# Performance work log

Measured on AMD Instinct MI355X. Metric: run time of the kernel, lower is better.

## Reference

```python
import jax, jax.numpy as jnp
import numpy as np
from functools import partial

VOCAB, D, H, L, T_MAX = 32000, 1024, 16, 8, 1024
HD = D // H
HIDDEN = int(D * 2.67)  # 2734, matches int(n_embd*hidden_mult)


def setup_inputs() -> dict:
    key = jax.random.key(0)
    ks = jax.random.split(key, 9)
    s = 0.02
    return {
        "idx": jax.random.randint(ks[0], (2, 1024), 0, VOCAB),
        "W_emb": jax.random.normal(ks[1], (VOCAB, D), jnp.float32) * s,  # tied with lm_head
        "norm1_w": jnp.ones((L, D), jnp.float32),
        "Wqkv": jax.random.normal(ks[2], (L, D, 3 * D), jnp.float32) * s,
        "Wout": jax.random.normal(ks[3], (L, D, D), jnp.float32) * s,
        "norm2_w": jnp.ones((L, D), jnp.float32),
        "Wg": jax.random.normal(ks[4], (L, D, HIDDEN), jnp.float32) * s,
        "Wu": jax.random.normal(ks[5], (L, D, HIDDEN), jnp.float32) * s,
        "Wd": jax.random.normal(ks[6], (L, HIDDEN, D), jnp.float32) * s,
        "final_norm_w": jnp.ones((D,), jnp.float32),
    }


def _rmsnorm(x, w, eps=1e-6):
    rms = jnp.sqrt(jnp.mean(x * x, axis=-1, keepdims=True) + eps)
    return x / rms * w


def _rope(x, cos_f, sin_f):
    # x: [B,H,T,hd]; cos_f/sin_f: [T, hd//2]
    x1, x2 = x[..., : HD // 2], x[..., HD // 2 :]
    c = cos_f[None, None]
    s = sin_f[None, None]
    return jnp.concatenate([x1 * c - x2 * s, x1 * s + x2 * c], axis=-1)


def _forward(idx, W_emb, norm1_w, Wqkv, Wout, norm2_w, Wg, Wu, Wd, final_norm_w):
    B, T = idx.shape
    # RoPE tables (buffers in the torch module)
    inv_freq = 1.0 / (10000.0 ** (jnp.arange(0, HD, 2, dtype=jnp.float32) / HD))
    ang = jnp.arange(T, dtype=jnp.float32)[:, None] * inv_freq[None, :]  # [T, hd//2]
    cos_f, sin_f = jnp.cos(ang), jnp.sin(ang)
    causal = jnp.tril(jnp.ones((T, T), dtype=bool))  # [T,T]
    scale = 1.0 / jnp.sqrt(jnp.float32(HD))

    def block(x, params):
        n1, wqkv, wout, n2, wg, wu, wd = params
        h = _rmsnorm(x, n1)
        qkv = (h @ wqkv).reshape(B, T, 3, H, HD).transpose(2, 0, 3, 1, 4)  # [3,B,H,T,hd]
        q, k, v = qkv[0], qkv[1], qkv[2]
        q = _rope(q, cos_f, sin_f)
        k = _rope(k, cos_f, sin_f)
        attn = jnp.einsum("bhqd,bhkd->bhqk", q, k) * scale
        attn = jnp.where(causal[None, None], attn, -jnp.inf)
        attn = jax.nn.softmax(attn, axis=-1)
        o = jnp.einsum("bhqk,bhkd->bhqd", attn, v)
        o = o.transpose(0, 2, 1, 3).reshape(B, T, D) @ wout
        x = x + o
        h2 = _rmsnorm(x, n2)
        x = x + (jax.nn.silu(h2 @ wg) * (h2 @ wu)) @ wd
        return x, None

    x = W_emb[idx]  # [B,T,D]
    x, _ = jax.lax.scan(block, x, (norm1_w, Wqkv, Wout, norm2_w, Wg, Wu, Wd))
    x = _rmsnorm(x, final_norm_w)
    return x @ W_emb.T  # tied lm_head -> [B,T,VOCAB]


def reference(idx, W_emb, norm1_w, Wqkv, Wout, norm2_w, Wg, Wu, Wd, final_norm_w):
    return _forward(idx, W_emb, norm1_w, Wqkv, Wout, norm2_w, Wg, Wu, Wd, final_norm_w)
```

## Files before the change

kernel.cpp:

```cpp
#include <hip/hip_runtime.h>
#include <cstdint>
#include <cmath>

#define D_MODEL 1024
#define T_SEQ   1024
#define NHEAD   16
#define NLAYER  8
#define HID     2734
#define HID_PAD 2816
#define NTOK    2048
#define VOCAB   32000

typedef __bf16 bf16x8 __attribute__((ext_vector_type(8)));
typedef __bf16 bf16x4 __attribute__((ext_vector_type(4)));
typedef float  f32x4  __attribute__((ext_vector_type(4)));

__device__ inline bf16x4 to_bf4(float a, float b, float c, float d) {
  bf16x4 t; t[0] = (__bf16)a; t[1] = (__bf16)b; t[2] = (__bf16)c; t[3] = (__bf16)d; return t;
}

__device__ inline void gload16(const __bf16* g, __bf16* l) {
  __builtin_amdgcn_global_load_lds(
      (const __attribute__((address_space(1))) void*)g,
      (__attribute__((address_space(3))) void*)l, 16, 0, 0);
}

__global__ __launch_bounds__(256) void embed_kernel(const int* __restrict__ idx,
                                                    const float* __restrict__ W,
                                                    float* __restrict__ x) {
  int t = blockIdx.x;
  int v = idx[t];
  float4 val = *(const float4*)&W[(size_t)v * D_MODEL + threadIdx.x * 4];
  *(float4*)&x[(size_t)t * D_MODEL + threadIdx.x * 4] = val;
}

__global__ __launch_bounds__(256) void rmsnorm_kernel(const float* __restrict__ x,
                                                      const float* __restrict__ w,
                                                      __bf16* __restrict__ out) {
  int row = blockIdx.x;
  int tid = threadIdx.x;
  float4 v = *(const float4*)&x[(size_t)row * D_MODEL + tid * 4];
  float s = v.x * v.x + v.y * v.y + v.z * v.z + v.w * v.w;
#pragma unroll
  for (int m = 32; m >= 1; m >>= 1) s += __shfl_xor(s, m, 64);
  __shared__ float red[4];
  if ((tid & 63) == 0) red[tid >> 6] = s;
  __syncthreads();
  float tot = red[0] + red[1] + red[2] + red[3];
  float inv = rsqrtf(tot * (1.0f / (float)D_MODEL) + 1e-6f);
  float4 wv = *(const float4*)&w[tid * 4];
  bf16x4 o4 = to_bf4(v.x * inv * wv.x, v.y * inv * wv.y, v.z * inv * wv.z, v.w * inv * wv.w);
  *(bf16x4*)&out[(size_t)row * D_MODEL + tid * 4] = o4;
}

__global__ __launch_bounds__(256) void rope_table_kernel(float* __restrict__ tab) {
  int p = blockIdx.x * 256 + threadIdx.x;
  int t = p >> 5, i = p & 31;
  float freq = exp2f(-(float)i * (13.287712379549449f / 32.0f));
  float sn, cs;
  sincosf((float)t * freq, &sn, &cs);
  tab[p] = cs;
  tab[32768 + p] = sn;
}

__global__ __launch_bounds__(256) void tp5_kernel(
    const float* __restrict__ Wqkv, const float* __restrict__ Wout,
    const float* __restrict__ Wg, const float* __restrict__ Wu,
    const float* __restrict__ Wd,
    __bf16* __restrict__ wqkvT, __bf16* __restrict__ woutT,
    __bf16* __restrict__ wguT, __bf16* __restrict__ wdT) {
  __shared__ __bf16 tile[64][65];
  int t = blockIdx.x;
  const float* in;
  __bf16* out;
  int R, C, Ro, rmul, roff, tr;
  if (t < 768)        { in = Wqkv; out = wqkvT; R = 1024; C = 3072; Ro = 1024; rmul = 1; roff = 0; tr = 16; }
  else if (t < 1024)  { t -= 768;  in = Wout; out = woutT; R = 1024; C = 1024; Ro = 1024; rmul = 1; roff = 0; tr = 16; }
  else if (t < 1728)  { t -= 1024; in = Wg; out = wguT; R = 1024; C = HID; Ro = 1024; rmul = 2; roff = 0; tr = 16; }
  else if (t < 2432)  { t -= 1728; in = Wu; out = wguT; R = 1024; C = HID; Ro = 1024; rmul = 2; roff = 1; tr = 16; }
  else                { t -= 2432; in = Wd; out = wdT; R = HID; C = 1024; Ro = HID_PAD; rmul = 1; roff = 0; tr = 44; }
  int r0 = (t % tr) * 64, c0 = (t / tr) * 64;
  int tid = threadIdx.x;
  bool fullc = (c0 + 64 <= C);
#pragma unroll
  for (int i = 0; i < 4; ++i) {
    int ri = i * 16 + (tid >> 4);
    int ci = (tid & 15) * 4;
    int r = r0 + ri;
    float4 v = {0.f, 0.f, 0.f, 0.f};
    if (r < R) {
      const float* p = in + (size_t)r * C + c0 + ci;
      if (fullc) {
        v = *(const float4*)p;
      } else {
        int c = c0 + ci;
        if (c + 0 < C) v.x = p[0];
        if (c + 1 < C) v.y = p[1];
        if (c + 2 < C) v.z = p[2];
        if (c + 3 < C) v.w = p[3];
      }
    }
    tile[ri][ci + 0] = (__bf16)v.x;
    tile[ri][ci + 1] = (__bf16)v.y;
    tile[ri][ci + 2] = (__bf16)v.z;
    tile[ri][ci + 3] = (__bf16)v.w;
  }
  __syncthreads();
#pragma unroll
  for (int i = 0; i < 4; ++i) {
    int oc = i * 16 + (tid >> 4);
    int orr = (tid & 15) * 4;
    bf16x4 tv;
    tv[0] = tile[orr + 0][oc];
    tv[1] = tile[orr + 1][oc];
    tv[2] = tile[orr + 2][oc];
    tv[3] = tile[orr + 3][oc];
    *(bf16x4*)&out[((size_t)(c0 + oc) * rmul + roff) * Ro + r0 + orr] = tv;
  }
}

__global__ __launch_bounds__(256) void convert_bf16_kernel(const float* __restrict__ in,
                                                           __bf16* __restrict__ out, int n4) {
  for (int i = blockIdx.x * 256 + threadIdx.x; i < n4; i += gridDim.x * 256) {
    float4 v = ((const float4*)in)[i];
    ((bf16x4*)out)[i] = to_bf4(v.x, v.y, v.z, v.w);
  }
}

template <int BM, int BN, int WM, int WN, int EPI>
__global__ __launch_bounds__(WM * WN * 64, 2) void gemm8(
    const __bf16* __restrict__ A, const __bf16* __restrict__ B,
    const float* __restrict__ Cin, void* __restrict__ Cout,
    int K, int ldc,
    const float* __restrict__ Tab, __bf16* __restrict__ Qr,
    __bf16* __restrict__ Kr, __bf16* __restrict__ Vt) {
  constexpr int NTH = WM * WN * 64;
  constexpr int MF = BM / (16 * WM);
  constexpr int MG = (MF + 3) / 4;
  constexpr int CL = (MF < 4) ? MF : 4;
  constexpr int LA = (BM * 4) / NTH;
  constexpr int LB = (BN * 4) / NTH;
  static_assert(BN / WN == 64, "NF must be 4");
  __shared__ __align__(16) __bf16 lds[(BM + BN) * 128];

  const int tid = threadIdx.x;
  const int lane = tid & 63, wid = tid >> 6;
  const int wr = wid / WN, wn = wid % WN;
  const int lr = lane & 15, lg = lane >> 4;

  const int gx = gridDim.x;
  const int nwg = gx * gridDim.y;
  const int orig = blockIdx.y * gx + blockIdx.x;
  const int q = nwg >> 3, r8 = nwg & 7;
  const int xcd = orig & 7, loc = orig >> 3;
  const int swz = ((xcd < r8) ? xcd * (q + 1) : r8 * (q + 1) + (xcd - r8) * q) + loc;
  const int brow = (swz % gx) * BM;
  const int bcol = (swz / gx) * BN;

  const __bf16* pAg[LA];
  const __bf16* pBg[LB];
  int opA[LA], opB[LB];
#pragma unroll
  for (int i = 0; i < LA; ++i) {
    int p = tid + i * NTH;
    int row = ((p >> 6) << 4) | (p & 15), j = (p >> 4) & 3;
    pAg[i] = A + (size_t)(brow + row) * K + j * 8;
    opA[i] = p * 8;
  }
#pragma unroll
  for (int i = 0; i < LB; ++i) {
    int p = tid + i * NTH;
    int row = ((p >> 6) << 4) | (p & 15), j = (p >> 4) & 3;
    pBg[i] = B + (size_t)(bcol + row) * K + j * 8;
    opB[i] = p * 8;
  }

  const int ntiles = K >> 6;

  auto STAGE_A = [&](int v, int kkq) {
    int vs = v < ntiles ? v : ntiles - 1;
    int ko = vs * 64 + kkq * 32;
    int sa = (v & 1) * (BM * 64) + kkq * (BM * 32);
#pragma unroll
    for (int i = 0; i < LA; ++i) gload16(pAg[i] + ko, lds + sa + opA[i]);
  };
  auto STAGE_B = [&](int v, int kkq) {
    int vs = v < ntiles ? v : ntiles - 1;
    int ko = vs * 64 + kkq * 32;
    int sb = BM * 128 + (v & 1) * (BN * 64) + kkq * (BN * 32);
#pragma unroll
    for (int i = 0; i < LB; ++i) gload16(pBg[i] + ko, lds + sb + opB[i]);
  };

  f32x4 acc[MF][4];
#pragma unroll
  for (int m = 0; m < MF; ++m)
#pragma unroll
    for (int n = 0; n < 4; ++n) acc[m][n] = (f32x4){0.f, 0.f, 0.f, 0.f};

  STAGE_A(0, 0); STAGE_B(0, 0);
  STAGE_A(0, 1); STAGE_B(0, 1);
  STAGE_A(1, 0); STAGE_B(1, 0);

  const int fragoff = lg * 128 + lr * 8;

  if constexpr (MF == 8) {
    for (int u = 0; u < ntiles; ++u) {
      const int buf = u & 1;
#pragma unroll
      for (int kk = 0; kk < 2; ++kk) {
        const int v = (kk == 0) ? u + 1 : u + 2;
        const int kkq = kk ^ 1;
        const __bf16* Ab = lds + buf * (BM * 64) + kk * (BM * 32);
        const __bf16* Bb = lds + BM * 128 + buf * (BN * 64) + kk * (BN * 32);
        asm volatile("s_waitcnt vmcnt(8)" ::: "memory");
        __builtin_amdgcn_sched_barrier(0);
        __builtin_amdgcn_s_barrier();
        __builtin_amdgcn_sched_barrier(0);
        STAGE_A(v, kkq);
        bf16x8 bfr[4], af0[4];
#pragma unroll
        for (int n = 0; n < 4; ++n)
          bfr[n] = *(const bf16x8*)(Bb + (wn * 64 + n * 16) * 32 + fragoff);
#pragma unroll
        for (int i = 0; i < 4; ++i)
          af0[i] = *(const bf16x8*)(Ab + (wr * 128 + i * 16) * 32 + fragoff);
        asm volatile("s_waitcnt lgkmcnt(0)" ::: "memory");
        __builtin_amdgcn_sched_barrier(0);
        __builtin_amdgcn_s_setprio(1);
#pragma unroll
        for (int i = 0; i < 4; ++i)
#pragma unroll
          for (int n = 0; n < 4; ++n)
            acc[i][n] = __builtin_amdgcn_mfma_f32_16x16x32_bf16(af0[i], bfr[n], acc[i][n], 0, 0, 0);
        __builtin_amdgcn_s_setprio(0);
        __builtin_amdgcn_s_barrier();
        STAGE_B(v, kkq);
        bf16x8 af1[4];
#pragma unroll
        for (int i = 0; i < 4; ++i)
          af1[i] = *(const bf16x8*)(Ab + (wr * 128 + 64 + i * 16) * 32 + fragoff);
        asm volatile("s_waitcnt lgkmcnt(0)" ::: "memory");
        __builtin_amdgcn_sched_barrier(0);
        __builtin_amdgcn_s_setprio(1);
#pragma unroll
        for (int i = 0; i < 4; ++i)
#pragma unroll
          for (int n = 0; n < 4; ++n)
            acc[4 + i][n] = __builtin_amdgcn_mfma_f32_16x16x32_bf16(af1[i], bfr[n], acc[4 + i][n], 0, 0, 0);
        __builtin_amdgcn_s_setprio(0);
        __builtin_amdgcn_s_barrier();
      }
    }
  } else {
    for (int u = 0; u < ntiles; ++u) {
      const int buf = u & 1;
#pragma unroll
      for (int kk = 0; kk < 2; ++kk) {
        if constexpr (LA + LB == 3) asm volatile("s_waitcnt vmcnt(6)" ::: "memory");
        else                        asm volatile("s_waitcnt vmcnt(8)" ::: "memory");
        __builtin_amdgcn_sched_barrier(0);
        __builtin_amdgcn_s_barrier();
        __builtin_amdgcn_sched_barrier(0);
        const int v = (kk == 0) ? u + 1 : u + 2;
        const int kkq = kk ^ 1;
        STAGE_A(v, kkq);
        STAGE_B(v, kkq);
        const __bf16* Ab = lds + buf * (BM * 64) + kk * (BM * 32);
        const __bf16* Bb = lds + BM * 128 + buf * (BN * 64) + kk * (BN * 32);
        bf16x8 bfr[4];
#pragma unroll
        for (int n = 0; n < 4; ++n)
          bfr[n] = *(const bf16x8*)(Bb + (wn * 64 + n * 16) * 32 + fragoff);
#pragma unroll
        for (int mg = 0; mg < MG; ++mg) {
          bf16x8 afr[CL];
#pragma unroll
          for (int i = 0; i < CL; ++i)
            afr[i] = *(const bf16x8*)(Ab + (wr * (BM / WM) + (mg * 4 + i) * 16) * 32 + fragoff);
          __builtin_amdgcn_s_setprio(1);
#pragma unroll
          for (int i = 0; i < CL; ++i)
#pragma unroll
            for (int n = 0; n < 4; ++n)
              acc[mg * 4 + i][n] =
                  __builtin_amdgcn_mfma_f32_16x16x32_bf16(afr[i], bfr[n], acc[mg * 4 + i][n], 0, 0, 0);
          __builtin_amdgcn_s_setprio(0);
        }
      }
    }
  }

  if constexpr (EPI == 5) {
    const int colw = bcol + wn * 64;
    const int secw = colw >> 10;
    const int h = (colw >> 6) & 15;
#pragma unroll
    for (int m = 0; m < MF; ++m) {
      int row0 = brow + wr * (BM / WM) + m * 16 + lg * 4;
      int bb = row0 >> 10;
      int t0 = row0 & 1023;
      int bh = bb * 16 + h;
      if (secw < 2) {
        __bf16* base = (secw == 0 ? Qr : Kr) + ((size_t)bh * T_SEQ + t0) * 64;
#pragma unroll
        for (int n = 0; n < 2; ++n) {
          int din = n * 16 + lr;
#pragma unroll
          for (int rr = 0; rr < 4; ++rr) {
            float a = acc[m][n][rr], b2 = acc[m][n + 2][rr];
            float cs = Tab[(t0 + rr) * 32 + din];
            float sn = Tab[32768 + (t0 + rr) * 32 + din];
            base[(size_t)rr * 64 + din]      = (__bf16)(a * cs - b2 * sn);
            base[(size_t)rr * 64 + din + 32] = (__bf16)(a * sn + b2 * cs);
          }
        }
      } else {
#pragma unroll
        for (int n = 0; n < 4; ++n) {
          int din = n * 16 + lr;
          bf16x4 pk;
#pragma unroll
          for (int rr = 0; rr < 4; ++rr) pk[rr] = (__bf16)acc[m][n][rr];
          *(bf16x4*)&Vt[((size_t)bh * 64 + din) * T_SEQ + t0] = pk;
        }
      }
    }
  } else {
#pragma unroll
    for (int m = 0; m < MF; ++m) {
#pragma unroll
      for (int n = 0; n < 4; ++n) {
#pragma unroll
        for (int rr = 0; rr < 4; ++rr) {
          int row = brow + wr * (BM / WM) + m * 16 + lg * 4 + rr;
          int col = bcol + wn * 64 + n * 16 + lr;
          size_t off = (size_t)row * ldc + col;
          float vv = acc[m][n][rr];
          if (EPI == 0) {
            ((float*)Cout)[off] = vv;
          } else if (EPI == 1) {
            ((float*)Cout)[off] = Cin[off] + vv;
          } else {
            float uv = __shfl_xor(vv, 1);
            if ((lr & 1) == 0) {
              float r = vv / (1.f + __expf(-vv)) * uv;
              ((__bf16*)Cout)[(size_t)row * ldc + (col >> 1)] = (__bf16)r;
            }
          }
        }
      }
    }
  }
}

__global__ __launch_bounds__(256) void attn_kernel(const __bf16* __restrict__ Qr,
                                                   const __bf16* __restrict__ Kr,
                                                   const __bf16* __restrict__ Vt,
                                                   __bf16* __restrict__ o) {
  __shared__ __align__(16) __bf16 lds[28672];
  const int tid = threadIdx.x;
  const int lane = tid & 63, w = tid >> 6;
  const int lr = lane & 15, lg = lane >> 4;
  const int bh = blockIdx.y, b = bh >> 4, h = bh & 15;
  const int qp = blockIdx.x;
  const __bf16* Kg = Kr + (size_t)bh * T_SEQ * 64;
  const __bf16* Vg = Vt + (size_t)bh * 64 * T_SEQ;
  const float scale = 0.125f;
  __bf16* Pw = lds + 20480 + w * 2048;

  for (int qs = 0; qs < 2; ++qs) {
    const int qb = qs ? (15 - qp) : qp;
    const int q0 = qb * 64;
    const __bf16* Qg = Qr + ((size_t)bh * T_SEQ + q0) * 64;

    __syncthreads();
    {
      int row = ((tid >> 6) << 4) | (tid & 15);
      int j = (tid >> 4) & 3;
      gload16(Qg + row * 64 + j * 8, lds + tid * 8);
      gload16(Qg + row * 64 + 32 + j * 8, lds + 2048 + tid * 8);
    }

    f32x4 accO[4];
#pragma unroll
    for (int n = 0; n < 4; ++n) accO[n] = (f32x4){0.f, 0.f, 0.f, 0.f};
    float mrow[4], lrow[4];
#pragma unroll
    for (int r = 0; r < 4; ++r) { mrow[r] = -1e30f; lrow[r] = 0.f; }

    const int ntile = ((q0 + 63) >> 7) + 1;

    for (int tt = 0; tt < ntile; ++tt) {
      const int j0 = tt * 128;
      __syncthreads();
#pragma unroll
      for (int i = 0; i < 2; ++i) {
        int p = tid + i * 256;
        int row = ((p >> 6) << 4) | (p & 15), j = (p >> 4) & 3;
        const __bf16* src = Kg + (size_t)(j0 + row) * 64 + j * 8;
        gload16(src, lds + 4096 + p * 8);
        gload16(src + 32, lds + 8192 + p * 8);
      }
#pragma unroll
      for (int s = 0; s < 4; ++s) {
        int d = ((tid >> 6) << 4) | (tid & 15), j = (tid >> 4) & 3;
        gload16(Vg + (size_t)d * T_SEQ + j0 + s * 32 + j * 8, lds + 12288 + s * 2048 + tid * 8);
      }
      __syncthreads();

      f32x4 s4[8];
#pragma unroll
      for (int n = 0; n < 8; ++n) s4[n] = (f32x4){0.f, 0.f, 0.f, 0.f};
#pragma unroll
      for (int kk = 0; kk < 2; ++kk) {
        bf16x8 aq = *(const bf16x8*)(lds + kk * 2048 + (w * 64 + lg * 16 + lr) * 8);
        __builtin_amdgcn_s_setprio(1);
#pragma unroll
        for (int jf = 0; jf < 8; ++jf) {
          bf16x8 bk = *(const bf16x8*)(lds + 4096 + kk * 4096 + (jf * 64 + lg * 16 + lr) * 8);
          s4[jf] = __builtin_amdgcn_mfma_f32_16x16x32_bf16(aq, bk, s4[jf], 0, 0, 0);
        }
        __builtin_amdgcn_s_setprio(0);
      }

      float pm[4];
#pragma unroll
      for (int r = 0; r < 4; ++r) pm[r] = -1e30f;
#pragma unroll
      for (int jf = 0; jf < 8; ++jf) {
        int gj = j0 + jf * 16 + lr;
#pragma unroll
        for (int r = 0; r < 4; ++r) {
          int gq = q0 + w * 16 + lg * 4 + r;
          float sv = s4[jf][r] * scale;
          if (gj > gq) sv = -1e30f;
          s4[jf][r] = sv;
          pm[r] = fmaxf(pm[r], sv);
        }
      }
#pragma unroll
      for (int r = 0; r < 4; ++r) {
#pragma unroll
        for (int m = 8; m >= 1; m >>= 1) pm[r] = fmaxf(pm[r], __shfl_xor(pm[r], m, 64));
      }
      float alpha[4];
#pragma unroll
      for (int r = 0; r < 4; ++r) {
        float mn = fmaxf(mrow[r], pm[r]);
        alpha[r] = expf(mrow[r] - mn);
        mrow[r] = mn;
      }
      float ps[4] = {0.f, 0.f, 0.f, 0.f};
#pragma unroll
      for (int jf = 0; jf < 8; ++jf) {
#pragma unroll
        for (int r = 0; r < 4; ++r) {
          float p = expf(s4[jf][r] - mrow[r]);
          s4[jf][r] = p;
          ps[r] += p;
        }
      }
#pragma unroll
      for (int r = 0; r < 4; ++r) {
#pragma unroll
        for (int m = 8; m >= 1; m >>= 1) ps[r] += __shfl_xor(ps[r], m, 64);
        lrow[r] = lrow[r] * alpha[r] + ps[r];
      }
#pragma unroll
      for (int n = 0; n < 4; ++n) {
#pragma unroll
        for (int r = 0; r < 4; ++r) accO[n][r] *= alpha[r];
      }

#pragma unroll
      for (int jf = 0; jf < 8; ++jf) {
        int s = jf >> 1;
        int rem = ((jf & 1) << 4) + lr;
        int base = s * 512 + (rem >> 3) * 128 + (rem & 7);
#pragma unroll
        for (int r = 0; r < 4; ++r) {
          int qloc = lg * 4 + r;
          Pw[base + qloc * 8] = (__bf16)s4[jf][r];
        }
      }
      asm volatile("s_waitcnt lgkmcnt(0)" ::: "memory");
      __builtin_amdgcn_sched_barrier(0);

#pragma unroll
      for (int s = 0; s < 4; ++s) {
        bf16x8 pa = *(const bf16x8*)(Pw + s * 512 + (lg * 16 + lr) * 8);
        __builtin_amdgcn_s_setprio(1);
#pragma unroll
        for (int nd = 0; nd < 4; ++nd) {
          bf16x8 bv = *(const bf16x8*)(lds + 12288 + s * 2048 + (nd * 64 + lg * 16 + lr) * 8);
          accO[nd] = __builtin_amdgcn_mfma_f32_16x16x32_bf16(pa, bv, accO[nd], 0, 0, 0);
        }
        __builtin_amdgcn_s_setprio(0);
      }
    }

#pragma unroll
    for (int nd = 0; nd < 4; ++nd) {
#pragma unroll
      for (int r = 0; r < 4; ++r) {
        int gq = q0 + w * 16 + lg * 4 + r;
        float val = accO[nd][r] / lrow[r];
        o[(size_t)(b * T_SEQ + gq) * D_MODEL + h * 64 + nd * 16 + lr] = (__bf16)val;
      }
    }
  }
}

extern "C" void kernel_launch(void* const* d_in, const int* in_sizes, int n_in,
                              void* d_out, int out_size, void* d_ws, size_t ws_size,
                              hipStream_t stream) {
  const int*   idx     = (const int*)d_in[0];
  const float* W_emb   = (const float*)d_in[1];
  const float* norm1_w = (const float*)d_in[2];
  const float* Wqkv    = (const float*)d_in[3];
  const float* Wout    = (const float*)d_in[4];
  const float* norm2_w = (const float*)d_in[5];
  const float* Wg      = (const float*)d_in[6];
  const float* Wu      = (const float*)d_in[7];
  const float* Wd      = (const float*)d_in[8];
  const float* fnorm   = (const float*)d_in[9];
  float* out = (float*)d_out;

  float*  x    = (float*)d_ws;
  float*  tab  = x + (size_t)NTOK * D_MODEL;
  __bf16* hb   = (__bf16*)(tab + 2 * 32768);
  __bf16* ob   = hb + (size_t)NTOK * D_MODEL;
  __bf16* ga   = ob + (size_t)NTOK * D_MODEL;
  __bf16* Qrb  = ga + (size_t)NTOK * HID_PAD;
  __bf16* Krb  = Qrb + (size_t)32 * T_SEQ * 64;
  __bf16* Vtb  = Krb + (size_t)32 * T_SEQ * 64;
  __bf16* wbuf = Vtb + (size_t)32 * T_SEQ * 64;

  __bf16* wqkvT = wbuf;
  __bf16* woutT = wqkvT + (size_t)3 * D_MODEL * D_MODEL;
  __bf16* wguT  = woutT + (size_t)D_MODEL * D_MODEL;
  __bf16* wdT   = wguT + (size_t)2 * HID_PAD * D_MODEL;

  embed_kernel<<<NTOK, 256, 0, stream>>>(idx, W_emb, x);
  rope_table_kernel<<<128, 256, 0, stream>>>(tab);

  for (int l = 0; l < NLAYER; ++l) {
    tp5_kernel<<<3136, 256, 0, stream>>>(
        Wqkv + (size_t)l * D_MODEL * 3 * D_MODEL,
        Wout + (size_t)l * D_MODEL * D_MODEL,
        Wg + (size_t)l * D_MODEL * HID,
        Wu + (size_t)l * D_MODEL * HID,
        Wd + (size_t)l * HID * D_MODEL,
        wqkvT, woutT, wguT, wdT);

    rmsnorm_kernel<<<NTOK, 256, 0, stream>>>(x, norm1_w + (size_t)l * D_MODEL, hb);
    gemm8<128, 256, 2, 4, 5><<<dim3(16, 12), 512, 0, stream>>>(
        hb, wqkvT, nullptr, nullptr, D_MODEL, 3 * D_MODEL, tab, Qrb, Krb, Vtb);
    attn_kernel<<<dim3(8, 32), 256, 0, stream>>>(Qrb, Krb, Vtb, ob);
    gemm8<128, 64, 4, 1, 1><<<dim3(16, 16), 256, 0, stream>>>(
        ob, woutT, x, x, D_MODEL, D_MODEL, nullptr, nullptr, nullptr, nullptr);
    rmsnorm_kernel<<<NTOK, 256, 0, stream>>>(x, norm2_w + (size_t)l * D_MODEL, hb);
    gemm8<256, 256, 2, 4, 4><<<dim3(8, 22), 512, 0, stream>>>(
        hb, wguT, nullptr, ga, D_MODEL, HID_PAD, nullptr, nullptr, nullptr, nullptr);
    gemm8<128, 64, 4, 1, 1><<<dim3(16, 16), 256, 0, stream>>>(
        ga, wdT, x, x, HID_PAD, D_MODEL, nullptr, nullptr, nullptr, nullptr);
  }

  rmsnorm_kernel<<<NTOK, 256, 0, stream>>>(x, fnorm, hb);
  convert_bf16_kernel<<<2048, 256, 0, stream>>>(W_emb, wbuf, VOCAB * D_MODEL / 4);
  gemm8<256, 256, 2, 4, 0><<<dim3(8, 125), 512, 0, stream>>>(
      hb, wbuf, nullptr, out, D_MODEL, VOCAB, nullptr, nullptr, nullptr, nullptr);
}
```

Baseline: 1.734 ms.

## Add triple-buffered 128x128 GEMM for QKV, gate/up and LM head

Adds a new GEMM kernel with 128x128 tiles, 4 waves and a three-slot LDS ring that prefetches two K-phases ahead. It replaces the 128x256 and 256x256 double-buffered GEMMs for QKV+RoPE, gate/up+SiLU and the LM head, giving more workgroups and allowing 3 blocks per CU. The aim is better CU occupancy and load balance on the 256-CU device. The trade-off is less data reuse per tile and more global traffic. The old gemm8 is kept only for the residual-add GEMMs.

```diff
diff --git a/kernel.cpp b/kernel.cpp
--- a/kernel.cpp
+++ b/kernel.cpp
@@ -127,13 +127,167 @@
   }
 }
 
-template <int BM, int BN, int WM, int WN, int EPI>
-__global__ __launch_bounds__(WM * WN * 64, 2) void gemm8(
+template <int WM, int WN, int EPI>
+__global__ __launch_bounds__(WM * WN * 64, 3) void gemmF(
     const __bf16* __restrict__ A, const __bf16* __restrict__ B,
     const float* __restrict__ Cin, void* __restrict__ Cout,
     int K, int ldc,
     const float* __restrict__ Tab, __bf16* __restrict__ Qr,
     __bf16* __restrict__ Kr, __bf16* __restrict__ Vt) {
+  constexpr int BM = WM * 64, BN = WN * 64;
+  constexpr int NTH = WM * WN * 64;
+  constexpr int SLOT = (BM + BN) * 32;
+  constexpr int LA = (BM * 32) / (NTH * 8);
+  constexpr int LB = (BN * 32) / (NTH * 8);
+  static_assert(LA + LB == 4, "vmcnt literal assumes 4 loads per stage event");
+  __shared__ __align__(16) __bf16 lds[3 * SLOT];
+
+  const int tid = threadIdx.x;
+  const int lane = tid & 63, wid = tid >> 6;
+  const int wr = wid / WN, wn = wid % WN;
+  const int lr = lane & 15, lg = lane >> 4;
+
+  const int gx = gridDim.x;
+  const int nwg = gx * gridDim.y;
+  const int orig = blockIdx.y * gx + blockIdx.x;
+  const int q = nwg >> 3, r8 = nwg & 7;
+  const int xcd = orig & 7, loc = orig >> 3;
+  const int swz = ((xcd < r8) ? xcd * (q + 1) : r8 * (q + 1) + (xcd - r8) * q) + loc;
+  const int brow = (swz % gx) * BM;
+  const int bcol = (swz / gx) * BN;
+
+  const __bf16* pAg[LA];
+  const __bf16* pBg[LB];
+  int opA[LA], opB[LB];
+#pragma unroll
+  for (int i = 0; i < LA; ++i) {
+    int p = tid + i * NTH;
+    int row = ((p >> 6) << 4) | (p & 15), j = (p >> 4) & 3;
+    pAg[i] = A + (size_t)(brow + row) * K + j * 8;
+    opA[i] = p * 8;
+  }
+#pragma unroll
+  for (int i = 0; i < LB; ++i) {
+    int p = tid + i * NTH;
+    int row = ((p >> 6) << 4) | (p & 15), j = (p >> 4) & 3;
+    pBg[i] = B + (size_t)(bcol + row) * K + j * 8;
+    opB[i] = BM * 32 + p * 8;
+  }
+
+  const int nph = K >> 5;
+
+  auto STAGE = [&](int ph) {
+    int ps = ph < nph ? ph : nph - 1;
+    int ko = ps * 32;
+    __bf16* s = lds + (ph % 3) * SLOT;
+#pragma unroll
+    for (int i = 0; i < LA; ++i) gload16(pAg[i] + ko, s + opA[i]);
+#pragma unroll
+    for (int i = 0; i < LB; ++i) gload16(pBg[i] + ko, s + opB[i]);
+  };
+
+  f32x4 acc[4][4];
+#pragma unroll
+  for (int m = 0; m < 4; ++m)
+#pragma unroll
+    for (int n = 0; n < 4; ++n) acc[m][n] = (f32x4){0.f, 0.f, 0.f, 0.f};
+
+  STAGE(0);
+  STAGE(1);
+
+  const int fragoff = lg * 128 + lr * 8;
+
+  for (int ph = 0; ph < nph; ++ph) {
+    asm volatile("s_waitcnt vmcnt(4)" ::: "memory");
+    __builtin_amdgcn_sched_barrier(0);
+    __builtin_amdgcn_s_barrier();
+    __builtin_amdgcn_sched_barrier(0);
+    STAGE(ph + 2);
+    const __bf16* Sb = lds + (ph % 3) * SLOT;
+    bf16x8 afr[4], bfr[4];
+#pragma unroll
+    for (int n = 0; n < 4; ++n)
+      bfr[n] = *(const bf16x8*)(Sb + BM * 32 + (wn * 64 + n * 16) * 32 + fragoff);
+#pragma unroll
+    for (int m = 0; m < 4; ++m)
+      afr[m] = *(const bf16x8*)(Sb + (wr * 64 + m * 16) * 32 + fragoff);
+    asm volatile("s_waitcnt lgkmcnt(0)" ::: "memory");
+    __builtin_amdgcn_sched_barrier(0);
+    __builtin_amdgcn_s_setprio(1);
+#pragma unroll
+    for (int m = 0; m < 4; ++m)
+#pragma unroll
+      for (int n = 0; n < 4; ++n)
+        acc[m][n] = __builtin_amdgcn_mfma_f32_16x16x32_bf16(afr[m], bfr[n], acc[m][n], 0, 0, 0);
+    __builtin_amdgcn_s_setprio(0);
+  }
+
+  if constexpr (EPI == 5) {
+    const int colw = bcol + wn * 64;
+    const int secw = colw >> 10;
+    const int h = (colw >> 6) & 15;
+#pragma unroll
+    for (int m = 0; m < 4; ++m) {
+      int row0 = brow + wr * 64 + m * 16 + lg * 4;
+      int bb = row0 >> 10;
+      int t0 = row0 & 1023;
+      int bh = bb * 16 + h;
+      if (secw < 2) {
+        __bf16* base = (secw == 0 ? Qr : Kr) + ((size_t)bh * T_SEQ + t0) * 64;
+#pragma unroll
+        for (int n = 0; n < 2; ++n) {
+          int din = n * 16 + lr;
+#pragma unroll
+          for (int rr = 0; rr < 4; ++rr) {
+            float a = acc[m][n][rr], b2 = acc[m][n + 2][rr];
+            float cs = Tab[(t0 + rr) * 32 + din];
+            float sn = Tab[32768 + (t0 + rr) * 32 + din];
+            base[(size_t)rr * 64 + din]      = (__bf16)(a * cs - b2 * sn);
+            base[(size_t)rr * 64 + din + 32] = (__bf16)(a * sn + b2 * cs);
+          }
+        }
+      } else {
+#pragma unroll
+        for (int n = 0; n < 4; ++n) {
+          int din = n * 16 + lr;
+          bf16x4 pk;
+#pragma unroll
+          for (int rr = 0; rr < 4; ++rr) pk[rr] = (__bf16)acc[m][n][rr];
+          *(bf16x4*)&Vt[((size_t)bh * 64 + din) * T_SEQ + t0] = pk;
+        }
+      }
+    }
+  } else {
+#pragma unroll
+    for (int m = 0; m < 4; ++m) {
+#pragma unroll
+      for (int n = 0; n < 4; ++n) {
+#pragma unroll
+        for (int rr = 0; rr < 4; ++rr) {
+          int row = brow + wr * 64 + m * 16 + lg * 4 + rr;
+          int col = bcol + wn * 64 + n * 16 + lr;
+          size_t off = (size_t)row * ldc + col;
+          float vv = acc[m][n][rr];
+          if (EPI == 0) {
+            ((float*)Cout)[off] = vv;
+          } else {
+            float uv = __shfl_xor(vv, 1);
+            if ((lr & 1) == 0) {
+              float r = vv / (1.f + __expf(-vv)) * uv;
+              ((__bf16*)Cout)[(size_t)row * ldc + (col >> 1)] = (__bf16)r;
+            }
+          }
+        }
+      }
+    }
+  }
+}
+
+template <int BM, int BN, int WM, int WN>
+__global__ __launch_bounds__(WM * WN * 64, 2) void gemm8(
+    const __bf16* __restrict__ A, const __bf16* __restrict__ B,
+    const float* __restrict__ Cin, float* __restrict__ Cout,
+    int K, int ldc) {
   constexpr int NTH = WM * WN * 64;
   constexpr int MF = BM / (16 * WM);
   constexpr int MG = (MF + 3) / 4;
@@ -204,151 +358,53 @@
 
   const int fragoff = lg * 128 + lr * 8;
 
-  if constexpr (MF == 8) {
-    for (int u = 0; u < ntiles; ++u) {
-      const int buf = u & 1;
-#pragma unroll
-      for (int kk = 0; kk < 2; ++kk) {
-        const int v = (kk == 0) ? u + 1 : u + 2;
-        const int kkq = kk ^ 1;
-        const __bf16* Ab = lds + buf * (BM * 64) + kk * (BM * 32);
-        const __bf16* Bb = lds + BM * 128 + buf * (BN * 64) + kk * (BN * 32);
-        asm volatile("s_waitcnt vmcnt(8)" ::: "memory");
-        __builtin_amdgcn_sched_barrier(0);
-        __builtin_amdgcn_s_barrier();
-        __builtin_amdgcn_sched_barrier(0);
-        STAGE_A(v, kkq);
-        bf16x8 bfr[4], af0[4];
-#pragma unroll
-        for (int n = 0; n < 4; ++n)
-          bfr[n] = *(const bf16x8*)(Bb + (wn * 64 + n * 16) * 32 + fragoff);
-#pragma unroll
-        for (int i = 0; i < 4; ++i)
-          af0[i] = *(const bf16x8*)(Ab + (wr * 128 + i * 16) * 32 + fragoff);
-        asm volatile("s_waitcnt lgkmcnt(0)" ::: "memory");
-        __builtin_amdgcn_sched_barrier(0);
+  for (int u = 0; u < ntiles; ++u) {
+    const int buf = u & 1;
+#pragma unroll
+    for (int kk = 0; kk < 2; ++kk) {
+      if constexpr (LA + LB == 3) asm volatile("s_waitcnt vmcnt(6)" ::: "memory");
+      else                        asm volatile("s_waitcnt vmcnt(8)" ::: "memory");
+      __builtin_amdgcn_sched_barrier(0);
+      __builtin_amdgcn_s_barrier();
+      __builtin_amdgcn_sched_barrier(0);
+      const int v = (kk == 0) ? u + 1 : u + 2;
+      const int kkq = kk ^ 1;
+      STAGE_A(v, kkq);
+      STAGE_B(v, kkq);
+      const __bf16* Ab = lds + buf * (BM * 64) + kk * (BM * 32);
+      const __bf16* Bb = lds + BM * 128 + buf * (BN * 64) + kk * (BN * 32);
+      bf16x8 bfr[4];
+#pragma unroll
+      for (int n = 0; n < 4; ++n)
+        bfr[n] = *(const bf16x8*)(Bb + (wn * 64 + n * 16) * 32 + fragoff);
+#pragma unroll
+      for (int mg = 0; mg < MG; ++mg) {
+        bf16x8 afr[CL];
+#pragma unroll
+        for (int i = 0; i < CL; ++i)
+          afr[i] = *(const bf16x8*)(Ab + (wr * (BM / WM) + (mg * 4 + i) * 16) * 32 + fragoff);
         __builtin_amdgcn_s_setprio(1);
 #pragma unroll
-        for (int i = 0; i < 4; ++i)
+        for (int i = 0; i < CL; ++i)
 #pragma unroll
           for (int n = 0; n < 4; ++n)
-            acc[i][n] = __builtin_amdgcn_mfma_f32_16x16x32_bf16(af0[i], bfr[n], acc[i][n], 0, 0, 0);
+            acc[mg * 4 + i][n] =
+                __builtin_amdgcn_mfma_f32_16x16x32_bf16(afr[i], bfr[n], acc[mg * 4 + i][n], 0, 0, 0);
         __builtin_amdgcn_s_setprio(0);
-        __builtin_amdgcn_s_barrier();
-        STAGE_B(v, kkq);
-        bf16x8 af1[4];
-#pragma unroll
-        for (int i = 0; i < 4; ++i)
-          af1[i] = *(const bf16x8*)(Ab + (wr * 128 + 64 + i * 16) * 32 + fragoff);
-        asm volatile("s_waitcnt lgkmcnt(0)" ::: "memory");
-        __builtin_amdgcn_sched_barrier(0);
-        __builtin_amdgcn_s_setprio(1);
-#pragma unroll
-        for (int i = 0; i < 4; ++i)
-#pragma unroll
-          for (int n = 0; n < 4; ++n)
-            acc[4 + i][n] = __builtin_amdgcn_mfma_f32_16x16x32_bf16(af1[i], bfr[n], acc[4 + i][n], 0, 0, 0);
-        __builtin_amdgcn_s_setprio(0);
-        __builtin_amdgcn_s_barrier();
-      }
-    }
-  } else {
-    for (int u = 0; u < ntiles; ++u) {
-      const int buf = u & 1;
-#pragma unroll
-      for (int kk = 0; kk < 2; ++kk) {
-        if constexpr (LA + LB == 3) asm volatile("s_waitcnt vmcnt(6)" ::: "memory");
-        else                        asm volatile("s_waitcnt vmcnt(8)" ::: "memory");
-        __builtin_amdgcn_sched_barrier(0);
-        __builtin_amdgcn_s_barrier();
-        __builtin_amdgcn_sched_barrier(0);
-        const int v = (kk == 0) ? u + 1 : u + 2;
-        const int kkq = kk ^ 1;
-        STAGE_A(v, kkq);
-        STAGE_B(v, kkq);
-        const __bf16* Ab = lds + buf * (BM * 64) + kk * (BM * 32);
-        const __bf16* Bb = lds + BM * 128 + buf * (BN * 64) + kk * (BN * 32);
-        bf16x8 bfr[4];
-#pragma unroll
-        for (int n = 0; n < 4; ++n)
-          bfr[n] = *(const bf16x8*)(Bb + (wn * 64 + n * 16) * 32 + fragoff);
-#pragma unroll
-        for (int mg = 0; mg < MG; ++mg) {
-          bf16x8 afr[CL];
-#pragma unroll
-          for (int i = 0; i < CL; ++i)
-            afr[i] = *(const bf16x8*)(Ab + (wr * (BM / WM) + (mg * 4 + i) * 16) * 32 + fragoff);
-          __builtin_amdgcn_s_setprio(1);
-#pragma unroll
-          for (int i = 0; i < CL; ++i)
-#pragma unroll
-            for (int n = 0; n < 4; ++n)
-              acc[mg * 4 + i][n] =
-                  __builtin_amdgcn_mfma_f32_16x16x32_bf16(afr[i], bfr[n], acc[mg * 4 + i][n], 0, 0, 0);
-          __builtin_amdgcn_s_setprio(0);
-        }
-      }
-    }
-  }
-
-  if constexpr (EPI == 5) {
-    const int colw = bcol + wn * 64;
-    const int secw = colw >> 10;
-    const int h = (colw >> 6) & 15;
-#pragma unroll
-    for (int m = 0; m < MF; ++m) {
-      int row0 = brow + wr * (BM / WM) + m * 16 + lg * 4;
-      int bb = row0 >> 10;
-      int t0 = row0 & 1023;
-      int bh = bb * 16 + h;
-      if (secw < 2) {
-        __bf16* base = (secw == 0 ? Qr : Kr) + ((size_t)bh * T_SEQ + t0) * 64;
-#pragma unroll
-        for (int n = 0; n < 2; ++n) {
-          int din = n * 16 + lr;
-#pragma unroll
-          for (int rr = 0; rr < 4; ++rr) {
-            float a = acc[m][n][rr], b2 = acc[m][n + 2][rr];
-            float cs = Tab[(t0 + rr) * 32 + din];
-            float sn = Tab[32768 + (t0 + rr) * 32 + din];
-            base[(size_t)rr * 64 + din]      = (__bf16)(a * cs - b2 * sn);
-            base[(size_t)rr * 64 + din + 32] = (__bf16)(a * sn + b2 * cs);
-          }
-        }
-      } else {
-#pragma unroll
-        for (int n = 0; n < 4; ++n) {
-          int din = n * 16 + lr;
-          bf16x4 pk;
-#pragma unroll
-          for (int rr = 0; rr < 4; ++rr) pk[rr] = (__bf16)acc[m][n][rr];
-          *(bf16x4*)&Vt[((size_t)bh * 64 + din) * T_SEQ + t0] = pk;
-        }
-      }
-    }
-  } else {
-#pragma unroll
-    for (int m = 0; m < MF; ++m) {
-#pragma unroll
-      for (int n = 0; n < 4; ++n) {
-#pragma unroll
-        for (int rr = 0; rr < 4; ++rr) {
-          int row = brow + wr * (BM / WM) + m * 16 + lg * 4 + rr;
-          int col = bcol + wn * 64 + n * 16 + lr;
-          size_t off = (size_t)row * ldc + col;
-          float vv = acc[m][n][rr];
-          if (EPI == 0) {
-            ((float*)Cout)[off] = vv;
-          } else if (EPI == 1) {
-            ((float*)Cout)[off] = Cin[off] + vv;
-          } else {
-            float uv = __shfl_xor(vv, 1);
-            if ((lr & 1) == 0) {
-              float r = vv / (1.f + __expf(-vv)) * uv;
-              ((__bf16*)Cout)[(size_t)row * ldc + (col >> 1)] = (__bf16)r;
-            }
-          }
-        }
+      }
+    }
+  }
+
+#pragma unroll
+  for (int m = 0; m < MF; ++m) {
+#pragma unroll
+    for (int n = 0; n < 4; ++n) {
+#pragma unroll
+      for (int rr = 0; rr < 4; ++rr) {
+        int row = brow + wr * (BM / WM) + m * 16 + lg * 4 + rr;
+        int col = bcol + wn * 64 + n * 16 + lr;
+        size_t off = (size_t)row * ldc + col;
+        Cout[off] = Cin[off] + acc[m][n][rr];
       }
     }
   }
@@ -555,20 +611,20 @@
         wqkvT, woutT, wguT, wdT);
 
     rmsnorm_kernel<<<NTOK, 256, 0, stream>>>(x, norm1_w + (size_t)l * D_MODEL, hb);
-    gemm8<128, 256, 2, 4, 5><<<dim3(16, 12), 512, 0, stream>>>(
+    gemmF<2, 2, 5><<<dim3(16, 24), 256, 0, stream>>>(
         hb, wqkvT, nullptr, nullptr, D_MODEL, 3 * D_MODEL, tab, Qrb, Krb, Vtb);
     attn_kernel<<<dim3(8, 32), 256, 0, stream>>>(Qrb, Krb, Vtb, ob);
-    gemm8<128, 64, 4, 1, 1><<<dim3(16, 16), 256, 0, stream>>>(
-        ob, woutT, x, x, D_MODEL, D_MODEL, nullptr, nullptr, nullptr, nullptr);
+    gemm8<128, 64, 4, 1><<<dim3(16, 16), 256, 0, stream>>>(
+        ob, woutT, x, x, D_MODEL, D_MODEL);
     rmsnorm_kernel<<<NTOK, 256, 0, stream>>>(x, norm2_w + (size_t)l * D_MODEL, hb);
-    gemm8<256, 256, 2, 4, 4><<<dim3(8, 22), 512, 0, stream>>>(
+    gemmF<2, 2, 4><<<dim3(16, 44), 256, 0, stream>>>(
         hb, wguT, nullptr, ga, D_MODEL, HID_PAD, nullptr, nullptr, nullptr, nullptr);
-    gemm8<128, 64, 4, 1, 1><<<dim3(16, 16), 256, 0, stream>>>(
-        ga, wdT, x, x, HID_PAD, D_MODEL, nullptr, nullptr, nullptr, nullptr);
+    gemm8<128, 64, 4, 1><<<dim3(16, 16), 256, 0, stream>>>(
+        ga, wdT, x, x, HID_PAD, D_MODEL);
   }
 
   rmsnorm_kernel<<<NTOK, 256, 0, stream>>>(x, fnorm, hb);
   convert_bf16_kernel<<<2048, 256, 0, stream>>>(W_emb, wbuf, VOCAB * D_MODEL / 4);
-  gemm8<256, 256, 2, 4, 0><<<dim3(8, 125), 512, 0, stream>>>(
+  gemmF<2, 2, 0><<<dim3(16, 250), 256, 0, stream>>>(
       hb, wbuf, nullptr, out, D_MODEL, VOCAB, nullptr, nullptr, nullptr, nullptr);
 }
```

Measured after the change: 1.943 ms. 12.1% more time.
